# Kernel optimization log

Measured on AMD Instinct MI355X. Metric: run time of the kernel, lower is better.

## Reference

```python
import jax, jax.numpy as jnp
import numpy as np

B, N, C = 256, 196, 768
H, HD = 12, 64          # num_heads, head_dim
WS = 14                 # window side, N = WS*WS
EPS = 1e-6


def setup_inputs() -> dict:
    key = jax.random.key(0)
    ks = jax.random.split(key, 7)
    s = 0.02
    return {
        "x": jax.random.normal(ks[0], (B, N, C), jnp.float32),
        "w_qkv": jax.random.normal(ks[1], (C, 3 * C), jnp.float32) * s,
        "pos_enc": jax.random.normal(ks[2], (1, N, C), jnp.float32) * s,
        "dwc_w": jax.random.normal(ks[3], (HD, 1, 5, 5), jnp.float32) * s,
        "dwc_b": jax.random.normal(ks[4], (HD,), jnp.float32) * s,
        "w_proj": jax.random.normal(ks[5], (C, C), jnp.float32) * s,
        "b_proj": jax.random.normal(ks[6], (C,), jnp.float32) * s,
    }


def _heads(t):
    # (B, N, C) -> (B*H, N, HD)   ['b n (h c) -> (b h) n c']
    return t.reshape(B, N, H, HD).transpose(0, 2, 1, 3).reshape(B * H, N, HD)


def reference(x, w_qkv, pos_enc, dwc_w, dwc_b, w_proj, b_proj):
    qkv = (x @ w_qkv).reshape(B, N, 3, C)
    q, k, v = qkv[:, :, 0], qkv[:, :, 1], qkv[:, :, 2]
    k = k + pos_enc
    # ReLU kernel feature map
    q = jax.nn.relu(q)
    k = jax.nn.relu(k)
    q, k, v = _heads(q), _heads(k), _heads(v)          # (BH, N, HD) each, fp32
    # normalizer z_i = 1 / (q_i . sum_j k_j + eps)
    z = 1.0 / (jnp.einsum("bic,bc->bi", q, k.sum(axis=1)) + EPS)
    # kv-first order (i*j*(c+d) > c*d*(i+j) for N=196, HD=64)
    kv = jnp.einsum("bjc,bjd->bcd", k, v)              # (BH, HD, HD)
    out = jnp.einsum("bic,bcd,bi->bid", q, kv, z)      # (BH, N, HD)
    # depthwise conv positional mixing on v
    fm = v.transpose(0, 2, 1).reshape(B * H, HD, WS, WS)  # 'b (w h) c -> b c w h'
    fm = jax.lax.conv_general_dilated(
        fm, dwc_w, window_strides=(1, 1), padding="SAME",
        dimension_numbers=("NCHW", "OIHW", "NCHW"), feature_group_count=HD,
    ) + dwc_b[None, :, None, None]
    fm = fm.reshape(B * H, HD, N).transpose(0, 2, 1)   # 'b c w h -> b (w h) c'
    out = out + fm
    # '(b h) n c -> b n (h c)'
    out = out.reshape(B, H, N, HD).transpose(0, 2, 1, 3).reshape(B, N, C)
    return out @ w_proj + b_proj
```

## Files before the change

### kernel.cpp

```cpp
#include <hip/hip_runtime.h>

typedef _Float16 half8_t __attribute__((ext_vector_type(8)));
typedef _Float16 half4_t __attribute__((ext_vector_type(4)));
typedef float f32x4 __attribute__((ext_vector_type(4)));

#define MFMA16(a, b, c) __builtin_amdgcn_mfma_f32_16x16x32_f16((a), (b), (c), 0, 0, 0)

typedef const unsigned int __attribute__((address_space(1)))* gas_ptr;
typedef unsigned int __attribute__((address_space(3)))* las_ptr;

__device__ __forceinline__ void gload16(const void* g, void* l) {
    __builtin_amdgcn_global_load_lds((gas_ptr)g, (las_ptr)l, 16, 0, 0);
}

__device__ __forceinline__ int xcd_swizzle(int bid, int nwg) {
    int xcd = bid & 7, i = bid >> 3;
    int q = nwg >> 3, r = nwg & 7;
    return (xcd < r ? xcd * (q + 1) : r * (q + 1) + (xcd - r) * q) + i;
}


__global__ void cvt_f2h_kernel(const float* __restrict__ in, _Float16* __restrict__ out, int n4) {
    int stride = gridDim.x * blockDim.x;
    for (int i = blockIdx.x * blockDim.x + threadIdx.x; i < n4; i += stride) {
        f32x4 v = *(const f32x4*)(in + (size_t)4 * i);
        half4_t h;
        h[0] = (_Float16)v[0]; h[1] = (_Float16)v[1];
        h[2] = (_Float16)v[2]; h[3] = (_Float16)v[3];
        *(half4_t*)(out + (size_t)4 * i) = h;
    }
}

__global__ void transpose768_kernel(const float* __restrict__ in, _Float16* __restrict__ out, int ncols) {
    int idx = blockIdx.x * 256 + threadIdx.x;
    int total = ncols * 768;
    if (idx < total) {
        int j = idx / 768;
        int k = idx - j * 768;
        out[idx] = (_Float16)in[(size_t)k * ncols + j];
    }
}


#define STG128(kof)                                                               \
    {                                                                             \
        _Pragma("unroll")                                                         \
        for (int i = 0; i < 4; ++i) {                                             \
            gload16(ArowS + (kof) + i * 24576, As + wave * 512 + i * 2048);       \
            gload16(BrowS + (kof) + i * 24576, Bs + wave * 512 + i * 2048);       \
        }                                                                         \
    }

__device__ __forceinline__ void run_gemm128(const _Float16* __restrict__ A,
                                            const _Float16* __restrict__ Bt,
                                            int mbase, int nbase,
                                            _Float16* As, _Float16* Bs,
                                            f32x4 (&acc)[4][4]) {
    const int tid = threadIdx.x;
    const int lane = tid & 63;
    const int wave = tid >> 6;
    const int wm = (wave >> 1) * 64;
    const int wn = (wave & 1) * 64;
    const int l15 = lane & 15;
    const int l4 = lane >> 4;
    const int rs = l15 & 7;
    const int srow = lane >> 3;
    const int ssl = ((lane & 7) ^ srow) << 3;

    #pragma unroll
    for (int mi = 0; mi < 4; ++mi)
        #pragma unroll
        for (int ni = 0; ni < 4; ++ni)
            acc[mi][ni] = (f32x4){0.f, 0.f, 0.f, 0.f};

    const _Float16* ArowS = A + (size_t)(mbase + wave * 8 + srow) * 768 + ssl;
    const _Float16* BrowS = Bt + (size_t)(nbase + wave * 8 + srow) * 768 + ssl;

    for (int kt = 0; kt < 12; ++kt) {
        STG128(kt * 64)
        __syncthreads();
        #pragma unroll
        for (int h = 0; h < 2; ++h) {
            half8_t a[4], b[4];
            #pragma unroll
            for (int mi = 0; mi < 4; ++mi)
                a[mi] = *(const half8_t*)(As + (wm + mi * 16 + l15) * 64 +
                                          (((h * 4 + l4) ^ rs) << 3));
            #pragma unroll
            for (int ni = 0; ni < 4; ++ni)
                b[ni] = *(const half8_t*)(Bs + (wn + ni * 16 + l15) * 64 +
                                          (((h * 4 + l4) ^ rs) << 3));
            #pragma unroll
            for (int mi = 0; mi < 4; ++mi)
                #pragma unroll
                for (int ni = 0; ni < 4; ++ni)
                    acc[mi][ni] = MFMA16(a[mi], b[ni], acc[mi][ni]);
        }
        __syncthreads();
    }
}

__global__ __launch_bounds__(256, 4) void gemm_qkv_kernel(
    const _Float16* __restrict__ xh, const _Float16* __restrict__ wqkvT,
    const float* __restrict__ pos_enc,
    _Float16* __restrict__ qh, _Float16* __restrict__ khT, _Float16* __restrict__ vhT) {
    __shared__ _Float16 As[8192];
    __shared__ _Float16 Bs[8192];
    int bid = blockIdx.x;
    int xcd = bid & 7, i = bid >> 3;
    int xq = xcd & 3, nhalf = xcd >> 2;
    int mtl = i / 9, ntl = i - mtl * 9;
    int mtile = xq * 98 + mtl;
    int ntile = nhalf * 9 + ntl;
    f32x4 acc[4][4];
    run_gemm128(xh, wqkvT, mtile * 128, ntile * 128, As, Bs, acc);

    const int tid = threadIdx.x;
    const int lane = tid & 63;
    const int wave = tid >> 6;
    const int wm = (wave >> 1) * 64;
    const int wn = (wave & 1) * 64;
    const int l15 = lane & 15;
    const int l4 = lane >> 4;

    const int s = ntile / 6;
    const int cb = (ntile - s * 6) * 128 + wn;

    if (s == 0) {
        #pragma unroll
        for (int mi = 0; mi < 4; ++mi) {
            #pragma unroll
            for (int ni = 0; ni < 4; ++ni) {
                int c = cb + ni * 16 + l15;
                int h = c >> 6, d = c & 63;
                #pragma unroll
                for (int r = 0; r < 4; ++r) {
                    int gr = mtile * 128 + wm + mi * 16 + l4 * 4 + r;
                    int b = gr / 196;
                    int n = gr - b * 196;
                    qh[((size_t)(b * 12 + h) * 196 + n) * 64 + d] =
                        (_Float16)fmaxf(acc[mi][ni][r], 0.f);
                }
            }
        }
    } else {
        _Float16* dstT = (s == 1) ? khT : vhT;
        #pragma unroll
        for (int mi = 0; mi < 4; ++mi) {
            int gr0 = mtile * 128 + wm + mi * 16 + l4 * 4;
            int b = gr0 / 196, n0 = gr0 - b * 196;
            #pragma unroll
            for (int ni = 0; ni < 4; ++ni) {
                int c = cb + ni * 16 + l15;
                int h = c >> 6, d = c & 63;
                half4_t w;
                #pragma unroll
                for (int r = 0; r < 4; ++r) {
                    float v = acc[mi][ni][r];
                    if (s == 1) { v += pos_enc[(n0 + r) * 768 + c]; v = fmaxf(v, 0.f); }
                    w[r] = (_Float16)v;
                }
                *(half4_t*)(dstT + ((size_t)(b * 12 + h) * 64 + d) * 196 + n0) = w;
            }
        }
    }
}

__global__ __launch_bounds__(256, 4) void gemm_proj_kernel(
    const _Float16* __restrict__ fused, const _Float16* __restrict__ wprojT,
    const float* __restrict__ b_proj, float* __restrict__ out) {
    __shared__ _Float16 As[8192];
    __shared__ _Float16 Bs[8192];
    int wgid = xcd_swizzle(blockIdx.x, 392 * 6);
    int mtile = wgid / 6, ntile = wgid - mtile * 6;
    f32x4 acc[4][4];
    run_gemm128(fused, wprojT, mtile * 128, ntile * 128, As, Bs, acc);

    const int tid = threadIdx.x;
    const int lane = tid & 63;
    const int wave = tid >> 6;
    const int wm = (wave >> 1) * 64;
    const int wn = (wave & 1) * 64;
    const int l15 = lane & 15;
    const int l4 = lane >> 4;

    #pragma unroll
    for (int mi = 0; mi < 4; ++mi) {
        #pragma unroll
        for (int ni = 0; ni < 4; ++ni) {
            int gc = ntile * 128 + wn + ni * 16 + l15;
            float bp = b_proj[gc];
            #pragma unroll
            for (int r = 0; r < 4; ++r) {
                int gr = mtile * 128 + wm + mi * 16 + l4 * 4 + r;
                out[(size_t)gr * 768 + gc] = acc[mi][ni][r] + bp;
            }
        }
    }
}

__global__ __launch_bounds__(512, 4) void attn_fused_kernel(
    const _Float16* __restrict__ qh, const _Float16* __restrict__ khT,
    const _Float16* __restrict__ vhT,
    const float* __restrict__ dwc_w, const float* __restrict__ dwc_b,
    _Float16* __restrict__ fused) {
    __shared__ _Float16 k_t[64 * 232];
    __shared__ _Float16 v_t[64 * 232];
    __shared__ _Float16 kv_l[64 * 64];
    __shared__ float ksum_p[512];
    __shared__ float ksum[64];
    __shared__ float zz[196];

    int bh = blockIdx.x;
    int bb = bh / 12, hh = bh - bb * 12;
    int tid = threadIdx.x;
    int lane = tid & 63, wave = tid >> 6;
    int l15 = lane & 15, l4 = lane >> 4;
    size_t base = (size_t)bh * 12544;

    for (int s = tid; s < 1856; s += 512) {
        int c = s / 29, g = s - c * 29;
        half8_t kk = {0, 0, 0, 0, 0, 0, 0, 0}, vv = {0, 0, 0, 0, 0, 0, 0, 0};
        const _Float16* kp = khT + base + c * 196 + g * 8;
        const _Float16* vp = vhT + base + c * 196 + g * 8;
        if (g < 24) {
            kk = *(const half8_t*)kp; vv = *(const half8_t*)vp;
        } else if (g == 24) {
            half4_t k4 = *(const half4_t*)kp, v4 = *(const half4_t*)vp;
            kk[0] = k4[0]; kk[1] = k4[1]; kk[2] = k4[2]; kk[3] = k4[3];
            vv[0] = v4[0]; vv[1] = v4[1]; vv[2] = v4[2]; vv[3] = v4[3];
        }
        *(half8_t*)(k_t + c * 232 + g * 8) = kk;
        *(half8_t*)(v_t + c * 232 + g * 8) = vv;
    }
    __syncthreads();

    {
        int ct = wave >> 1, dt0 = (wave & 1) * 2;
        f32x4 acc0 = {0.f, 0.f, 0.f, 0.f}, acc1 = {0.f, 0.f, 0.f, 0.f};
        #pragma unroll
        for (int ks = 0; ks < 7; ++ks) {
            half8_t a  = *(const half8_t*)(k_t + (ct * 16 + l15) * 232 + ks * 32 + l4 * 8);
            half8_t b0 = *(const half8_t*)(v_t + (dt0 * 16 + l15) * 232 + ks * 32 + l4 * 8);
            half8_t b1 = *(const half8_t*)(v_t + (dt0 * 16 + 16 + l15) * 232 + ks * 32 + l4 * 8);
            acc0 = MFMA16(a, b0, acc0);
            acc1 = MFMA16(a, b1, acc1);
        }
        half4_t h0, h1;
        #pragma unroll
        for (int r = 0; r < 4; ++r) { h0[r] = (_Float16)acc0[r]; h1[r] = (_Float16)acc1[r]; }
        int slot = ct * 2 + (l4 >> 1), sub = (l4 & 1) * 4;
        int d0 = dt0 * 16 + l15, d1 = d0 + 16;
        *(half4_t*)(kv_l + d0 * 64 + (((slot ^ (d0 & 7)) << 3) + sub)) = h0;
        *(half4_t*)(kv_l + d1 * 64 + (((slot ^ (d1 & 7)) << 3) + sub)) = h1;
    }
    {
        int n0 = wave * 25;
        int n1 = (n0 + 25 < 196) ? (n0 + 25) : 196;
        float s = 0.f;
        for (int n = n0; n < n1; ++n) s += (float)k_t[lane * 232 + n];
        ksum_p[wave * 64 + lane] = s;
    }
    __syncthreads();
    if (tid < 64) {
        float s = 0.f;
        #pragma unroll
        for (int w = 0; w < 8; ++w) s += ksum_p[w * 64 + tid];
        ksum[tid] = s;
    }
    __syncthreads();
    if (tid < 196) {
        const _Float16* qrow = qh + base + tid * 64;
        float s = 0.f;
        #pragma unroll
        for (int c8 = 0; c8 < 8; ++c8) {
            half8_t qv = *(const half8_t*)(qrow + c8 * 8);
            #pragma unroll
            for (int j = 0; j < 8; ++j) s += (float)qv[j] * ksum[c8 * 8 + j];
        }
        zz[tid] = 1.0f / (s + 1e-6f);
    }
    __syncthreads();

    for (int t = wave; t < 52; t += 8) {
        int mt = t >> 2, dt = t & 3;
        int d = dt * 16 + l15;
        f32x4 acc = {0.f, 0.f, 0.f, 0.f};
        const _Float16* qrow = qh + base + (mt * 16 + l15) * 64;
        half8_t a0 = *(const half8_t*)(qrow + l4 * 8);
        half8_t a1 = *(const half8_t*)(qrow + 32 + l4 * 8);
        half8_t b0 = *(const half8_t*)(kv_l + d * 64 + ((l4 ^ (d & 7)) << 3));
        half8_t b1 = *(const half8_t*)(kv_l + d * 64 + (((l4 + 4) ^ (d & 7)) << 3));
        acc = MFMA16(a0, b0, acc);
        acc = MFMA16(a1, b1, acc);

        float bd = dwc_b[d];
        float wc[25];
        #pragma unroll
        for (int j2 = 0; j2 < 25; ++j2) wc[j2] = dwc_w[d * 25 + j2];

        #pragma unroll
        for (int r = 0; r < 4; ++r) {
            int i = mt * 16 + l4 * 4 + r;
            if (i < 196) {
                int y = i / 14, x2 = i - y * 14;
                float cacc = bd;
                #pragma unroll
                for (int ky = 0; ky < 5; ++ky) {
                    int yy = y + ky - 2;
                    bool oky = (unsigned)yy < 14u;
                    #pragma unroll
                    for (int kx = 0; kx < 5; ++kx) {
                        int xx = x2 + kx - 2;
                        if (oky && (unsigned)xx < 14u)
                            cacc += (float)v_t[d * 232 + (yy * 14 + xx)] * wc[ky * 5 + kx];
                    }
                }
                float res = acc[r] * zz[i] + cacc;
                fused[((size_t)bb * 196 + i) * 768 + hh * 64 + d] = (_Float16)res;
            }
        }
    }
}


extern "C" void kernel_launch(void* const* d_in, const int* in_sizes, int n_in,
                              void* d_out, int out_size, void* d_ws, size_t ws_size,
                              hipStream_t stream) {
    const float* x       = (const float*)d_in[0];
    const float* w_qkv   = (const float*)d_in[1];
    const float* pos_enc = (const float*)d_in[2];
    const float* dwc_w   = (const float*)d_in[3];
    const float* dwc_b   = (const float*)d_in[4];
    const float* w_proj  = (const float*)d_in[5];
    const float* b_proj  = (const float*)d_in[6];

    const size_t NEEDED = 340574208;
    if (ws_size < NEEDED) return;

    char* ws = (char*)d_ws;
    _Float16* xh     = (_Float16*)(ws + 0);
    _Float16* fused  = xh;
    _Float16* wqkvT  = (_Float16*)(ws + 77070336);
    _Float16* wprojT = (_Float16*)(ws + 80609280);
    _Float16* qh     = (_Float16*)(ws + 81788928);
    _Float16* khT    = (_Float16*)(ws + 158859264);
    _Float16* vhT    = (_Float16*)(ws + 235929600);

    cvt_f2h_kernel<<<4096, 256, 0, stream>>>(x, xh, 9633792);
    transpose768_kernel<<<(2304 * 768 + 255) / 256, 256, 0, stream>>>(w_qkv, wqkvT, 2304);
    transpose768_kernel<<<(768 * 768 + 255) / 256, 256, 0, stream>>>(w_proj, wprojT, 768);
    gemm_qkv_kernel<<<392 * 18, 256, 0, stream>>>(xh, wqkvT, pos_enc, qh, khT, vhT);
    attn_fused_kernel<<<3072, 512, 0, stream>>>(qh, khT, vhT, dwc_w, dwc_b, fused);
    gemm_proj_kernel<<<392 * 6, 256, 0, stream>>>(fused, wprojT, b_proj, (float*)d_out);
}
```

Before: 616.9 us.

## Pad K/V transposed rows to 224 and restructure attention kernel without LDS staging

The QKV GEMM now writes transposed K and V with a row stride of 224 and zero-fills the tail, so the attention kernel can read MFMA operands directly from global memory instead of staging K and V in shared memory. The key sum is computed with wave shuffles, and the depthwise conv is reorganized so each thread handles one output row per channel, reusing loaded V rows across kernel taps. The scaled attention output goes through a small LDS buffer before being combined with the conv. Dropping the large LDS arrays allows a higher occupancy hint, at the cost of more global traffic from direct loads and a larger workspace footprint for the padded K/V.

```diff
diff --git a/kernel.cpp b/kernel.cpp
--- a/kernel.cpp
+++ b/kernel.cpp
@@ -2,6 +2,7 @@
 
 typedef _Float16 half8_t __attribute__((ext_vector_type(8)));
 typedef _Float16 half4_t __attribute__((ext_vector_type(4)));
+typedef _Float16 half2_t __attribute__((ext_vector_type(2)));
 typedef float f32x4 __attribute__((ext_vector_type(4)));
 
 #define MFMA16(a, b, c) __builtin_amdgcn_mfma_f32_16x16x32_f16((a), (b), (c), 0, 0, 0)
@@ -153,6 +154,7 @@
             for (int ni = 0; ni < 4; ++ni) {
                 int c = cb + ni * 16 + l15;
                 int h = c >> 6, d = c & 63;
+                _Float16* row = dstT + ((size_t)(b * 12 + h) * 64 + d) * 224;
                 half4_t w;
                 #pragma unroll
                 for (int r = 0; r < 4; ++r) {
@@ -160,7 +162,12 @@
                     if (s == 1) { v += pos_enc[(n0 + r) * 768 + c]; v = fmaxf(v, 0.f); }
                     w[r] = (_Float16)v;
                 }
-                *(half4_t*)(dstT + ((size_t)(b * 12 + h) * 64 + d) * 196 + n0) = w;
+                *(half4_t*)(row + n0) = w;
+                if (n0 == 192) {
+                    half4_t z4 = {(_Float16)0.f, (_Float16)0.f, (_Float16)0.f, (_Float16)0.f};
+                    #pragma unroll
+                    for (int p = 196; p < 224; p += 4) *(half4_t*)(row + p) = z4;
+                }
             }
         }
     }
@@ -199,15 +206,13 @@
     }
 }
 
-__global__ __launch_bounds__(512, 4) void attn_fused_kernel(
+__global__ __launch_bounds__(512, 6) void attn_fused_kernel(
     const _Float16* __restrict__ qh, const _Float16* __restrict__ khT,
     const _Float16* __restrict__ vhT,
     const float* __restrict__ dwc_w, const float* __restrict__ dwc_b,
     _Float16* __restrict__ fused) {
-    __shared__ _Float16 k_t[64 * 232];
-    __shared__ _Float16 v_t[64 * 232];
     __shared__ _Float16 kv_l[64 * 64];
-    __shared__ float ksum_p[512];
+    __shared__ _Float16 pv[64 * 236];
     __shared__ float ksum[64];
     __shared__ float zz[196];
 
@@ -216,33 +221,33 @@
     int tid = threadIdx.x;
     int lane = tid & 63, wave = tid >> 6;
     int l15 = lane & 15, l4 = lane >> 4;
-    size_t base = (size_t)bh * 12544;
-
-    for (int s = tid; s < 1856; s += 512) {
-        int c = s / 29, g = s - c * 29;
-        half8_t kk = {0, 0, 0, 0, 0, 0, 0, 0}, vv = {0, 0, 0, 0, 0, 0, 0, 0};
-        const _Float16* kp = khT + base + c * 196 + g * 8;
-        const _Float16* vp = vhT + base + c * 196 + g * 8;
-        if (g < 24) {
-            kk = *(const half8_t*)kp; vv = *(const half8_t*)vp;
-        } else if (g == 24) {
-            half4_t k4 = *(const half4_t*)kp, v4 = *(const half4_t*)vp;
-            kk[0] = k4[0]; kk[1] = k4[1]; kk[2] = k4[2]; kk[3] = k4[3];
-            vv[0] = v4[0]; vv[1] = v4[1]; vv[2] = v4[2]; vv[3] = v4[3];
-        }
-        *(half8_t*)(k_t + c * 232 + g * 8) = kk;
-        *(half8_t*)(v_t + c * 232 + g * 8) = vv;
-    }
-    __syncthreads();
+    size_t kbase = (size_t)bh * 14336;
+    size_t qbase = (size_t)bh * 12544;
+
+    #pragma unroll
+    for (int j = 0; j < 8; ++j) {
+        int c = wave * 8 + j;
+        float s = 0.f;
+        if (lane < 49) {
+            half4_t kq = *(const half4_t*)(khT + kbase + c * 224 + lane * 4);
+            s = (float)kq[0] + (float)kq[1] + (float)kq[2] + (float)kq[3];
+        }
+        #pragma unroll
+        for (int off = 32; off; off >>= 1) s += __shfl_down(s, off);
+        if (lane == 0) ksum[c] = s;
+    }
 
     {
         int ct = wave >> 1, dt0 = (wave & 1) * 2;
+        const _Float16* ka  = khT + kbase + (ct * 16 + l15) * 224 + l4 * 8;
+        const _Float16* vb0 = vhT + kbase + (dt0 * 16 + l15) * 224 + l4 * 8;
+        const _Float16* vb1 = vb0 + 16 * 224;
         f32x4 acc0 = {0.f, 0.f, 0.f, 0.f}, acc1 = {0.f, 0.f, 0.f, 0.f};
         #pragma unroll
         for (int ks = 0; ks < 7; ++ks) {
-            half8_t a  = *(const half8_t*)(k_t + (ct * 16 + l15) * 232 + ks * 32 + l4 * 8);
-            half8_t b0 = *(const half8_t*)(v_t + (dt0 * 16 + l15) * 232 + ks * 32 + l4 * 8);
-            half8_t b1 = *(const half8_t*)(v_t + (dt0 * 16 + 16 + l15) * 232 + ks * 32 + l4 * 8);
+            half8_t a  = *(const half8_t*)(ka + ks * 32);
+            half8_t b0 = *(const half8_t*)(vb0 + ks * 32);
+            half8_t b1 = *(const half8_t*)(vb1 + ks * 32);
             acc0 = MFMA16(a, b0, acc0);
             acc1 = MFMA16(a, b1, acc1);
         }
@@ -254,23 +259,10 @@
         *(half4_t*)(kv_l + d0 * 64 + (((slot ^ (d0 & 7)) << 3) + sub)) = h0;
         *(half4_t*)(kv_l + d1 * 64 + (((slot ^ (d1 & 7)) << 3) + sub)) = h1;
     }
-    {
-        int n0 = wave * 25;
-        int n1 = (n0 + 25 < 196) ? (n0 + 25) : 196;
-        float s = 0.f;
-        for (int n = n0; n < n1; ++n) s += (float)k_t[lane * 232 + n];
-        ksum_p[wave * 64 + lane] = s;
-    }
     __syncthreads();
-    if (tid < 64) {
-        float s = 0.f;
-        #pragma unroll
-        for (int w = 0; w < 8; ++w) s += ksum_p[w * 64 + tid];
-        ksum[tid] = s;
-    }
-    __syncthreads();
+
     if (tid < 196) {
-        const _Float16* qrow = qh + base + tid * 64;
+        const _Float16* qrow = qh + qbase + tid * 64;
         float s = 0.f;
         #pragma unroll
         for (int c8 = 0; c8 < 8; ++c8) {
@@ -286,38 +278,64 @@
         int mt = t >> 2, dt = t & 3;
         int d = dt * 16 + l15;
         f32x4 acc = {0.f, 0.f, 0.f, 0.f};
-        const _Float16* qrow = qh + base + (mt * 16 + l15) * 64;
+        const _Float16* qrow = qh + qbase + (mt * 16 + l15) * 64;
         half8_t a0 = *(const half8_t*)(qrow + l4 * 8);
         half8_t a1 = *(const half8_t*)(qrow + 32 + l4 * 8);
         half8_t b0 = *(const half8_t*)(kv_l + d * 64 + ((l4 ^ (d & 7)) << 3));
         half8_t b1 = *(const half8_t*)(kv_l + d * 64 + (((l4 + 4) ^ (d & 7)) << 3));
         acc = MFMA16(a0, b0, acc);
         acc = MFMA16(a1, b1, acc);
-
-        float bd = dwc_b[d];
-        float wc[25];
-        #pragma unroll
-        for (int j2 = 0; j2 < 25; ++j2) wc[j2] = dwc_w[d * 25 + j2];
-
+        int i0 = mt * 16 + l4 * 4;
+        half4_t w;
         #pragma unroll
         for (int r = 0; r < 4; ++r) {
-            int i = mt * 16 + l4 * 4 + r;
-            if (i < 196) {
-                int y = i / 14, x2 = i - y * 14;
-                float cacc = bd;
-                #pragma unroll
-                for (int ky = 0; ky < 5; ++ky) {
-                    int yy = y + ky - 2;
-                    bool oky = (unsigned)yy < 14u;
+            int i = i0 + r;
+            w[r] = (_Float16)(acc[r] * ((i < 196) ? zz[i] : 0.f));
+        }
+        *(half4_t*)(pv + d * 236 + i0) = w;
+    }
+    __syncthreads();
+
+    #pragma unroll
+    for (int rnd = 0; rnd < 2; ++rnd) {
+        int y = rnd * 8 + wave;
+        int d = lane;
+        if (y < 14) {
+            float cacc[14];
+            float bd = dwc_b[d];
+            #pragma unroll
+            for (int x = 0; x < 14; ++x) cacc[x] = bd;
+            const float* wrow = dwc_w + d * 25;
+            #pragma unroll
+            for (int ky = 0; ky < 5; ++ky) {
+                int yy = y + ky - 2;
+                if ((unsigned)yy < 14u) {
+                    const _Float16* vr = vhT + kbase + d * 224 + yy * 14;
+                    float hv[14];
+                    #pragma unroll
+                    for (int u = 0; u < 7; ++u) {
+                        half2_t w2 = *(const half2_t*)(vr + u * 2);
+                        hv[2 * u] = (float)w2[0];
+                        hv[2 * u + 1] = (float)w2[1];
+                    }
                     #pragma unroll
                     for (int kx = 0; kx < 5; ++kx) {
-                        int xx = x2 + kx - 2;
-                        if (oky && (unsigned)xx < 14u)
-                            cacc += (float)v_t[d * 232 + (yy * 14 + xx)] * wc[ky * 5 + kx];
+                        float wk = wrow[ky * 5 + kx];
+                        #pragma unroll
+                        for (int x = 0; x < 14; ++x) {
+                            int c = x + kx - 2;
+                            if (c >= 0 && c < 14) cacc[x] += hv[c] * wk;
+                        }
                     }
                 }
-                float res = acc[r] * zz[i] + cacc;
-                fused[((size_t)bb * 196 + i) * 768 + hh * 64 + d] = (_Float16)res;
+            }
+            int ibase = y * 14;
+            _Float16* orow = fused + ((size_t)bb * 196 + ibase) * 768 + hh * 64 + d;
+            #pragma unroll
+            for (int xp = 0; xp < 7; ++xp) {
+                half2_t pw = *(const half2_t*)(pv + d * 236 + ibase + 2 * xp);
+                orow[(2 * xp) * 768]     = (_Float16)((float)pw[0] + cacc[2 * xp]);
+                orow[(2 * xp + 1) * 768] = (_Float16)((float)pw[1] + cacc[2 * xp + 1]);
             }
         }
     }
@@ -345,7 +363,7 @@
     _Float16* wprojT = (_Float16*)(ws + 80609280);
     _Float16* qh     = (_Float16*)(ws + 81788928);
     _Float16* khT    = (_Float16*)(ws + 158859264);
-    _Float16* vhT    = (_Float16*)(ws + 235929600);
+    _Float16* vhT    = (_Float16*)(ws + 246939648);
 
     cvt_f2h_kernel<<<4096, 256, 0, stream>>>(x, xh, 9633792);
     transpose768_kernel<<<(2304 * 768 + 255) / 256, 256, 0, stream>>>(w_qkv, wqkvT, 2304);
```

Result: faster. 580.2 us (-5.9%).
